# Performance work log

Hardware: AMD Instinct MI355X
Metric: run time of the kernel (lower is better)

The kernel has to match this reference:

```python
import jax, jax.numpy as jnp
import numpy as np


def setup_inputs() -> dict:
    key = jax.random.key(0)
    k1, k2 = jax.random.split(key)
    B, C, H, W = 8, 19, 512, 1024
    preds = jax.random.normal(k1, (B, C, H, W), dtype=jnp.float32)
    targets = jax.random.randint(k2, (B, H, W), 0, C, dtype=jnp.int32)
    return {"preds": preds, "targets": targets}


def reference(preds, targets):
    # preds: [B, C, H, W] logits; targets: [B, H, W] int class labels
    C = preds.shape[1]
    # softmax over class dim (does not change argmax but kept for faithfulness)
    probs = jax.nn.softmax(preds, axis=1)
    pred_lab = jnp.argmax(probs, axis=1)  # [B, H, W]

    p = pred_lab.ravel().astype(jnp.int32)
    t = targets.ravel().astype(jnp.int32)

    # single-pass histograms replacing the per-class Python loop
    pred_count = jnp.bincount(p, length=C)                      # |pred == c|
    true_count = jnp.bincount(t, length=C)                      # |true == c|
    # intersection: count matches routed to their class, mismatches to bin C
    inter = jnp.bincount(jnp.where(p == t, p, C), length=C + 1)[:C]

    union = pred_count + true_count - inter
    iou_all = jnp.where(
        true_count > 0,
        inter.astype(jnp.float32) / jnp.maximum(union, 1).astype(jnp.float32),
        jnp.float32(0.0),
    )
    # original loop iterates classes 1..C-1 (skips class 0 / background)
    iou = iou_all[1:]
    mean_iou = jnp.mean(iou)
    return iou, mean_iou
```

## Files before the change

### kernel.cpp

```cpp
#include <hip/hip_runtime.h>

#define NCLASS 19
#define HW (512 * 1024)
#define NB 8
#define NPIX (NB * HW)
#define NGROUP (NPIX / 4)
#define GROUPS_PER_BLOCK 512
#define GRID (NGROUP / GROUPS_PER_BLOCK)

typedef float v4f __attribute__((ext_vector_type(4)));
typedef int   v4i __attribute__((ext_vector_type(4)));


__global__ __launch_bounds__(256) void iou_count_kernel(
    const float* __restrict__ preds,
    const int* __restrict__ targets,
    unsigned int* __restrict__ g_pred,
    unsigned int* __restrict__ g_true,
    unsigned int* __restrict__ g_inter)
{
    __shared__ unsigned int s_pred[NCLASS];
    __shared__ unsigned int s_true[NCLASS];
    __shared__ unsigned int s_inter[NCLASS];

    const int t = threadIdx.x;
    if (t < NCLASS) { s_pred[t] = 0u; s_true[t] = 0u; s_inter[t] = 0u; }
    __syncthreads();

    const int gblk = blockIdx.x * GROUPS_PER_BLOCK;
    const int p0   = gblk << 2;
    const int b    = p0 >> 19;
    const int hw   = p0 & (HW - 1);

    const v4f* __restrict__ base =
        (const v4f*)(preds + (size_t)b * NCLASS * HW + hw) + t;
    const size_t plane4 = HW / 4;

    v4f m0 = __builtin_nontemporal_load(&base[0]);
    v4f m1 = __builtin_nontemporal_load(&base[256]);
    int i0x = 0, i0y = 0, i0z = 0, i0w = 0;
    int i1x = 0, i1y = 0, i1z = 0, i1w = 0;

    #pragma unroll
    for (int c = 1; c < NCLASS; ++c) {
        const v4f a = __builtin_nontemporal_load(&base[(size_t)c * plane4]);
        const v4f d = __builtin_nontemporal_load(&base[(size_t)c * plane4 + 256]);
        if (a.x > m0.x) { m0.x = a.x; i0x = c; }
        if (a.y > m0.y) { m0.y = a.y; i0y = c; }
        if (a.z > m0.z) { m0.z = a.z; i0z = c; }
        if (a.w > m0.w) { m0.w = a.w; i0w = c; }
        if (d.x > m1.x) { m1.x = d.x; i1x = c; }
        if (d.y > m1.y) { m1.y = d.y; i1y = c; }
        if (d.z > m1.z) { m1.z = d.z; i1z = c; }
        if (d.w > m1.w) { m1.w = d.w; i1w = c; }
    }

    const v4i* __restrict__ tgt4 = (const v4i*)targets + gblk + t;
    const v4i ta = __builtin_nontemporal_load(&tgt4[0]);
    const v4i tb = __builtin_nontemporal_load(&tgt4[256]);

    atomicAdd(&s_pred[i0x], 1u);
    atomicAdd(&s_pred[i0y], 1u);
    atomicAdd(&s_pred[i0z], 1u);
    atomicAdd(&s_pred[i0w], 1u);
    atomicAdd(&s_pred[i1x], 1u);
    atomicAdd(&s_pred[i1y], 1u);
    atomicAdd(&s_pred[i1z], 1u);
    atomicAdd(&s_pred[i1w], 1u);

    atomicAdd(&s_true[ta.x], 1u);
    atomicAdd(&s_true[ta.y], 1u);
    atomicAdd(&s_true[ta.z], 1u);
    atomicAdd(&s_true[ta.w], 1u);
    atomicAdd(&s_true[tb.x], 1u);
    atomicAdd(&s_true[tb.y], 1u);
    atomicAdd(&s_true[tb.z], 1u);
    atomicAdd(&s_true[tb.w], 1u);

    if (i0x == ta.x) atomicAdd(&s_inter[i0x], 1u);
    if (i0y == ta.y) atomicAdd(&s_inter[i0y], 1u);
    if (i0z == ta.z) atomicAdd(&s_inter[i0z], 1u);
    if (i0w == ta.w) atomicAdd(&s_inter[i0w], 1u);
    if (i1x == tb.x) atomicAdd(&s_inter[i1x], 1u);
    if (i1y == tb.y) atomicAdd(&s_inter[i1y], 1u);
    if (i1z == tb.z) atomicAdd(&s_inter[i1z], 1u);
    if (i1w == tb.w) atomicAdd(&s_inter[i1w], 1u);

    __syncthreads();
    if (t < NCLASS) {
        if (s_pred[t])  atomicAdd(&g_pred[t],  s_pred[t]);
        if (s_true[t])  atomicAdd(&g_true[t],  s_true[t]);
        if (s_inter[t]) atomicAdd(&g_inter[t], s_inter[t]);
    }
}

__global__ void iou_finalize_kernel(
    const unsigned int* __restrict__ g_pred,
    const unsigned int* __restrict__ g_true,
    const unsigned int* __restrict__ g_inter,
    float* __restrict__ out)
{
    __shared__ float s_iou[NCLASS];
    const int t = threadIdx.x;
    if (t < NCLASS) {
        const unsigned int pc = g_pred[t];
        const unsigned int tc = g_true[t];
        const unsigned int ic = g_inter[t];
        const unsigned int un = pc + tc - ic;
        const unsigned int und = un > 1u ? un : 1u;
        const float iou = (tc > 0u) ? ((float)ic / (float)und) : 0.0f;
        s_iou[t] = iou;
        if (t >= 1) out[t - 1] = iou;
    }
    __syncthreads();
    if (t == 0) {
        float s = 0.0f;
        for (int c = 1; c < NCLASS; ++c) s += s_iou[c];
        out[NCLASS - 1] = s / (float)(NCLASS - 1);
    }
}

extern "C" void kernel_launch(void* const* d_in, const int* in_sizes, int n_in,
                              void* d_out, int out_size, void* d_ws, size_t ws_size,
                              hipStream_t stream) {
    const float* preds  = (const float*)d_in[0];
    const int* targets  = (const int*)d_in[1];
    float* out          = (float*)d_out;

    unsigned int* g_pred  = (unsigned int*)d_ws;
    unsigned int* g_true  = g_pred + NCLASS;
    unsigned int* g_inter = g_true + NCLASS;

    hipMemsetAsync(d_ws, 0, 3 * NCLASS * sizeof(unsigned int), stream);

    iou_count_kernel<<<GRID, 256, 0, stream>>>(preds, targets,
                                               g_pred, g_true, g_inter);
    iou_finalize_kernel<<<1, 64, 0, stream>>>(g_pred, g_true, g_inter, out);
}
```

Measured before the change: 433.3 us.

## Replace global atomics with per-block partial histograms reduced in finalize

Each count block now writes its 57 shared-memory counts to a per-block slot in a class-major partials array, where before it issued global atomicAdds on three 19-entry histograms. The finalize kernel grows to 1024 threads and reduces the 2048 partials per counter with vector loads and a shared-memory tree. The memset launch is no longer needed. This removes contention on a few hot global addresses and one launch, at the cost of extra workspace writes and a larger single-block reduction.

Measured after the change: 403.6 us. -6.9%, faster.

```diff
diff --git a/kernel.cpp b/kernel.cpp
--- a/kernel.cpp
+++ b/kernel.cpp
@@ -1,6 +1,7 @@
 #include <hip/hip_runtime.h>
 
 #define NCLASS 19
+#define NCNT   (3 * NCLASS)
 #define HW (512 * 1024)
 #define NB 8
 #define NPIX (NB * HW)
@@ -10,21 +11,18 @@
 
 typedef float v4f __attribute__((ext_vector_type(4)));
 typedef int   v4i __attribute__((ext_vector_type(4)));
+typedef unsigned int v4u __attribute__((ext_vector_type(4)));
 
 
 __global__ __launch_bounds__(256) void iou_count_kernel(
     const float* __restrict__ preds,
     const int* __restrict__ targets,
-    unsigned int* __restrict__ g_pred,
-    unsigned int* __restrict__ g_true,
-    unsigned int* __restrict__ g_inter)
+    unsigned int* __restrict__ partials)
 {
-    __shared__ unsigned int s_pred[NCLASS];
-    __shared__ unsigned int s_true[NCLASS];
-    __shared__ unsigned int s_inter[NCLASS];
+    __shared__ unsigned int s_cnt[NCNT];
 
     const int t = threadIdx.x;
-    if (t < NCLASS) { s_pred[t] = 0u; s_true[t] = 0u; s_inter[t] = 0u; }
+    if (t < NCNT) s_cnt[t] = 0u;
     __syncthreads();
 
     const int gblk = blockIdx.x * GROUPS_PER_BLOCK;
@@ -59,53 +57,72 @@
     const v4i ta = __builtin_nontemporal_load(&tgt4[0]);
     const v4i tb = __builtin_nontemporal_load(&tgt4[256]);
 
-    atomicAdd(&s_pred[i0x], 1u);
-    atomicAdd(&s_pred[i0y], 1u);
-    atomicAdd(&s_pred[i0z], 1u);
-    atomicAdd(&s_pred[i0w], 1u);
-    atomicAdd(&s_pred[i1x], 1u);
-    atomicAdd(&s_pred[i1y], 1u);
-    atomicAdd(&s_pred[i1z], 1u);
-    atomicAdd(&s_pred[i1w], 1u);
+    atomicAdd(&s_cnt[i0x], 1u);
+    atomicAdd(&s_cnt[i0y], 1u);
+    atomicAdd(&s_cnt[i0z], 1u);
+    atomicAdd(&s_cnt[i0w], 1u);
+    atomicAdd(&s_cnt[i1x], 1u);
+    atomicAdd(&s_cnt[i1y], 1u);
+    atomicAdd(&s_cnt[i1z], 1u);
+    atomicAdd(&s_cnt[i1w], 1u);
 
-    atomicAdd(&s_true[ta.x], 1u);
-    atomicAdd(&s_true[ta.y], 1u);
-    atomicAdd(&s_true[ta.z], 1u);
-    atomicAdd(&s_true[ta.w], 1u);
-    atomicAdd(&s_true[tb.x], 1u);
-    atomicAdd(&s_true[tb.y], 1u);
-    atomicAdd(&s_true[tb.z], 1u);
-    atomicAdd(&s_true[tb.w], 1u);
+    atomicAdd(&s_cnt[NCLASS + ta.x], 1u);
+    atomicAdd(&s_cnt[NCLASS + ta.y], 1u);
+    atomicAdd(&s_cnt[NCLASS + ta.z], 1u);
+    atomicAdd(&s_cnt[NCLASS + ta.w], 1u);
+    atomicAdd(&s_cnt[NCLASS + tb.x], 1u);
+    atomicAdd(&s_cnt[NCLASS + tb.y], 1u);
+    atomicAdd(&s_cnt[NCLASS + tb.z], 1u);
+    atomicAdd(&s_cnt[NCLASS + tb.w], 1u);
 
-    if (i0x == ta.x) atomicAdd(&s_inter[i0x], 1u);
-    if (i0y == ta.y) atomicAdd(&s_inter[i0y], 1u);
-    if (i0z == ta.z) atomicAdd(&s_inter[i0z], 1u);
-    if (i0w == ta.w) atomicAdd(&s_inter[i0w], 1u);
-    if (i1x == tb.x) atomicAdd(&s_inter[i1x], 1u);
-    if (i1y == tb.y) atomicAdd(&s_inter[i1y], 1u);
-    if (i1z == tb.z) atomicAdd(&s_inter[i1z], 1u);
-    if (i1w == tb.w) atomicAdd(&s_inter[i1w], 1u);
+    if (i0x == ta.x) atomicAdd(&s_cnt[2 * NCLASS + i0x], 1u);
+    if (i0y == ta.y) atomicAdd(&s_cnt[2 * NCLASS + i0y], 1u);
+    if (i0z == ta.z) atomicAdd(&s_cnt[2 * NCLASS + i0z], 1u);
+    if (i0w == ta.w) atomicAdd(&s_cnt[2 * NCLASS + i0w], 1u);
+    if (i1x == tb.x) atomicAdd(&s_cnt[2 * NCLASS + i1x], 1u);
+    if (i1y == tb.y) atomicAdd(&s_cnt[2 * NCLASS + i1y], 1u);
+    if (i1z == tb.z) atomicAdd(&s_cnt[2 * NCLASS + i1z], 1u);
+    if (i1w == tb.w) atomicAdd(&s_cnt[2 * NCLASS + i1w], 1u);
 
     __syncthreads();
-    if (t < NCLASS) {
-        if (s_pred[t])  atomicAdd(&g_pred[t],  s_pred[t]);
-        if (s_true[t])  atomicAdd(&g_true[t],  s_true[t]);
-        if (s_inter[t]) atomicAdd(&g_inter[t], s_inter[t]);
-    }
+    if (t < NCNT) partials[t * GRID + blockIdx.x] = s_cnt[t];
 }
 
-__global__ void iou_finalize_kernel(
-    const unsigned int* __restrict__ g_pred,
-    const unsigned int* __restrict__ g_true,
-    const unsigned int* __restrict__ g_inter,
+__global__ __launch_bounds__(1024) void iou_finalize_kernel(
+    const unsigned int* __restrict__ partials,
     float* __restrict__ out)
 {
+    __shared__ unsigned int s_red[NCNT][16];
+    __shared__ unsigned int s_tot[NCNT];
     __shared__ float s_iou[NCLASS];
+
     const int t = threadIdx.x;
+    const int j = t >> 4;
+    const int k = t & 15;
+
+    if (j < NCNT) {
+        const v4u* __restrict__ p4 = (const v4u*)(partials + j * GRID);
+        unsigned int s = 0;
+        #pragma unroll
+        for (int i = 0; i < 32; ++i) {
+            const v4u v = p4[i * 16 + k];
+            s += v.x + v.y + v.z + v.w;
+        }
+        s_red[j][k] = s;
+    }
+    __syncthreads();
+    if (j < NCNT && k == 0) {
+        unsigned int s = 0;
+        #pragma unroll
+        for (int i = 0; i < 16; ++i) s += s_red[j][i];
+        s_tot[j] = s;
+    }
+    __syncthreads();
+
     if (t < NCLASS) {
-        const unsigned int pc = g_pred[t];
-        const unsigned int tc = g_true[t];
-        const unsigned int ic = g_inter[t];
+        const unsigned int pc = s_tot[t];
+        const unsigned int tc = s_tot[NCLASS + t];
+        const unsigned int ic = s_tot[2 * NCLASS + t];
         const unsigned int un = pc + tc - ic;
         const unsigned int und = un > 1u ? un : 1u;
         const float iou = (tc > 0u) ? ((float)ic / (float)und) : 0.0f;
@@ -126,14 +143,8 @@
     const float* preds  = (const float*)d_in[0];
     const int* targets  = (const int*)d_in[1];
     float* out          = (float*)d_out;
+    unsigned int* partials = (unsigned int*)d_ws;
 
-    unsigned int* g_pred  = (unsigned int*)d_ws;
-    unsigned int* g_true  = g_pred + NCLASS;
-    unsigned int* g_inter = g_true + NCLASS;
-
-    hipMemsetAsync(d_ws, 0, 3 * NCLASS * sizeof(unsigned int), stream);
-
-    iou_count_kernel<<<GRID, 256, 0, stream>>>(preds, targets,
-                                               g_pred, g_true, g_inter);
-    iou_finalize_kernel<<<1, 64, 0, stream>>>(g_pred, g_true, g_inter, out);
+    iou_count_kernel<<<GRID, 256, 0, stream>>>(preds, targets, partials);
+    iou_finalize_kernel<<<1, 1024, 0, stream>>>(partials, out);
 }
```
